# Kernel tuning notes

Hardware: AMD Instinct MI355X
Metric: run time of the kernel (lower is better)

Reference implementation:

```python
import jax, jax.numpy as jnp
import numpy as np

B, T, S, I, H = 128, 256, 256, 512, 512


def setup_inputs() -> dict:
    key = jax.random.key(0)
    ks = jax.random.split(key, 10)
    sc = 0.02
    return {
        "x": jax.random.normal(ks[0], (B, T, I), jnp.float32),
        "h0": jax.random.normal(ks[1], (B, H), jnp.float32),
        "c0": jax.random.normal(ks[2], (B, H), jnp.float32),
        "ctx": jax.random.normal(ks[3], (S, B, H), jnp.float32),
        "Wi": jax.random.normal(ks[4], (4 * H, I), jnp.float32) * sc,
        "bi": jax.random.normal(ks[5], (4 * H,), jnp.float32) * sc,
        "Wh": jax.random.normal(ks[6], (4 * H, H), jnp.float32) * sc,
        "bh": jax.random.normal(ks[7], (4 * H,), jnp.float32) * sc,
        "W_in": jax.random.normal(ks[8], (H, H), jnp.float32) * sc,
        "W_out": jax.random.normal(ks[9], (H, 2 * H), jnp.float32) * sc,
    }


def reference(x, h0, c0, ctx, Wi, bi, Wh, bh, W_in, W_out):
    ctx_b = jnp.transpose(ctx, (1, 0, 2))  # [B, S, H]

    def step(carry, xt):
        hx, cx = carry
        gates = xt @ Wi.T + bi + hx @ Wh.T + bh  # [B, 4H]
        i_g, f_g, g_g, o_g = jnp.split(gates, 4, axis=1)
        cy = jax.nn.sigmoid(f_g) * cx + jax.nn.sigmoid(i_g) * jnp.tanh(g_g)
        hy = jax.nn.sigmoid(o_g) * jnp.tanh(cy)
        # soft dot attention
        target = hy @ W_in.T                              # [B, H]
        attn = jax.nn.softmax(jnp.einsum('bsh,bh->bs', ctx_b, target), axis=1)
        wc = jnp.einsum('bs,bsh->bh', attn, ctx_b)        # [B, H]
        h_tilde = jnp.tanh(jnp.concatenate([wc, hy], axis=1) @ W_out.T)
        return (h_tilde, cy), h_tilde

    (hf, cf), outs = jax.lax.scan(step, (h0, c0), jnp.transpose(x, (1, 0, 2)))
    output = jnp.transpose(outs, (1, 0, 2))  # [B, T, H] (batch_first)
    return output, hf, cf
```

## Files before the change

### kernel.cpp

```cpp
#include <hip/hip_runtime.h>
#include <hip/hip_bf16.h>
#include <stdint.h>

#define B_ 128
#define T_ 256
#define S_ 256
#define I_ 512
#define H_ 512
#define RSLOT 32

typedef __attribute__((ext_vector_type(8))) short short8;
typedef __attribute__((ext_vector_type(4))) float f32x4;
typedef unsigned short ushort_t;

__device__ __forceinline__ float bf2f(ushort_t u){
  union{ unsigned int i; float f;} v; v.i = ((unsigned int)u)<<16; return v.f;
}
__device__ __forceinline__ ushort_t f2bf(float f){
  union{ unsigned int i; float f;} v; v.f=f;
  unsigned int x=v.i; unsigned int r = x + 0x7fffu + ((x>>16)&1u);
  return (ushort_t)(r>>16);
}
__device__ __forceinline__ float sigm(float x){ return 1.f/(1.f + __expf(-x)); }
__device__ __forceinline__ float tanh_s(float x){
  float a = fabsf(x);
  float e = __expf(-2.f*a);
  float t = (1.f - e)/(1.f + e);
  return x < 0.f ? -t : t;
}

__device__ __forceinline__ f32x4 MFMA16(short8 a, short8 b, f32x4 c){
  typedef __attribute__((ext_vector_type(8))) __bf16 bf16x8;
  return __builtin_amdgcn_mfma_f32_16x16x32_bf16(
      __builtin_bit_cast(bf16x8, a), __builtin_bit_cast(bf16x8, b), c, 0, 0, 0);
}

__device__ __forceinline__ void fab_store_u64(ushort_t* p, unsigned long long v){
  __hip_atomic_store((unsigned long long*)p, v, __ATOMIC_RELAXED, __HIP_MEMORY_SCOPE_AGENT);
}


__global__ void k_cvt_bf16(const float* __restrict__ src, ushort_t* __restrict__ dst, int n){
  int i = (blockIdx.x*blockDim.x + threadIdx.x)*4;
  int stride = gridDim.x*blockDim.x*4;
  for (; i < n; i += stride){
    float4 v = *(const float4*)(src + i);
    ushort4 o; o.x=f2bf(v.x); o.y=f2bf(v.y); o.z=f2bf(v.z); o.w=f2bf(v.w);
    *(ushort4*)(dst + i) = o;
  }
}

__global__ void k_relayout_ctx(const float* __restrict__ ctx, ushort_t* __restrict__ ctxb){
  int s = blockIdx.x >> 7;
  int b = blockIdx.x & 127;
  int h4 = threadIdx.x * 4;
  float4 v = *(const float4*)(ctx + ((size_t)s*128 + b)*512 + h4);
  ushort4 o; o.x=f2bf(v.x); o.y=f2bf(v.y); o.z=f2bf(v.z); o.w=f2bf(v.w);
  *(ushort4*)(ctxb + ((size_t)b*256 + s)*512 + h4) = o;
}

__global__ void k_transpose_512(const float* __restrict__ in, float* __restrict__ out){
  __shared__ float tile[32][33];
  int bx = blockIdx.x*32, by = blockIdx.y*32;
  int tx = threadIdx.x, ty = threadIdx.y;
  for (int r=0;r<32;r+=8) tile[ty+r][tx] = in[(by+ty+r)*512 + bx+tx];
  __syncthreads();
  for (int r=0;r<32;r+=8) out[(bx+ty+r)*512 + by+tx] = tile[tx][ty+r];
}

__global__ void k_init_state(const float* __restrict__ h0, const float* __restrict__ c0,
                             ushort_t* __restrict__ hring0, float* __restrict__ cyb){
  int i = blockIdx.x*blockDim.x + threadIdx.x;
  hring0[i] = f2bf(h0[i]);
  cyb[i] = c0[i];
}

__global__ void k_zero_bar(int* f){
  if (threadIdx.x < 256) f[threadIdx.x] = 0;
}

template<int BIAS, int SWAP>
__global__ __launch_bounds__(256) void k_gemm_bt(
    const float* __restrict__ A, const float* __restrict__ Bm,
    ushort_t* __restrict__ C, int M, int N, int K,
    const float* __restrict__ bias0, const float* __restrict__ bias1){
  __shared__ ushort_t Asm[128][40];
  __shared__ ushort_t Bsm[128][40];
  const int tid = threadIdx.x;
  const int mBase = blockIdx.x*128, nBase = blockIdx.y*128;
  const int l = tid & 63, wv = tid >> 6;
  const int wm = (wv>>1)*64, wn = (wv&1)*64;
  const int lr = l & 15, lq = l >> 4;
  const int srow = tid >> 1, scol = (tid & 1)*16;
  const float* Ap = A + (size_t)(mBase + srow)*K + scol;
  const float* Bp = Bm + (size_t)(nBase + srow)*K + scol;

  f32x4 acc[4][4];
  #pragma unroll
  for (int i=0;i<4;i++)
    #pragma unroll
    for (int j=0;j<4;j++) acc[i][j] = (f32x4)0.f;

  for (int k0 = 0; k0 < K; k0 += 32){
    float4 a0 = *(const float4*)(Ap + k0);
    float4 a1 = *(const float4*)(Ap + k0 + 4);
    float4 a2 = *(const float4*)(Ap + k0 + 8);
    float4 a3 = *(const float4*)(Ap + k0 + 12);
    float4 b0 = *(const float4*)(Bp + k0);
    float4 b1 = *(const float4*)(Bp + k0 + 4);
    float4 b2 = *(const float4*)(Bp + k0 + 8);
    float4 b3 = *(const float4*)(Bp + k0 + 12);
    __syncthreads();
    {
      ushort4 w;
      w.x=f2bf(a0.x); w.y=f2bf(a0.y); w.z=f2bf(a0.z); w.w=f2bf(a0.w);
      *(ushort4*)&Asm[srow][scol+0]  = w;
      w.x=f2bf(a1.x); w.y=f2bf(a1.y); w.z=f2bf(a1.z); w.w=f2bf(a1.w);
      *(ushort4*)&Asm[srow][scol+4]  = w;
      w.x=f2bf(a2.x); w.y=f2bf(a2.y); w.z=f2bf(a2.z); w.w=f2bf(a2.w);
      *(ushort4*)&Asm[srow][scol+8]  = w;
      w.x=f2bf(a3.x); w.y=f2bf(a3.y); w.z=f2bf(a3.z); w.w=f2bf(a3.w);
      *(ushort4*)&Asm[srow][scol+12] = w;
      w.x=f2bf(b0.x); w.y=f2bf(b0.y); w.z=f2bf(b0.z); w.w=f2bf(b0.w);
      *(ushort4*)&Bsm[srow][scol+0]  = w;
      w.x=f2bf(b1.x); w.y=f2bf(b1.y); w.z=f2bf(b1.z); w.w=f2bf(b1.w);
      *(ushort4*)&Bsm[srow][scol+4]  = w;
      w.x=f2bf(b2.x); w.y=f2bf(b2.y); w.z=f2bf(b2.z); w.w=f2bf(b2.w);
      *(ushort4*)&Bsm[srow][scol+8]  = w;
      w.x=f2bf(b3.x); w.y=f2bf(b3.y); w.z=f2bf(b3.z); w.w=f2bf(b3.w);
      *(ushort4*)&Bsm[srow][scol+12] = w;
    }
    __syncthreads();
    short8 aF[4], bF[4];
    #pragma unroll
    for (int i=0;i<4;i++) aF[i] = *(const short8*)&Asm[wm + i*16 + lr][lq*8];
    #pragma unroll
    for (int j=0;j<4;j++) bF[j] = *(const short8*)&Bsm[wn + j*16 + lr][lq*8];
    #pragma unroll
    for (int i=0;i<4;i++)
      #pragma unroll
      for (int j=0;j<4;j++)
        acc[i][j] = MFMA16(aF[i], bF[j], acc[i][j]);
  }

  #pragma unroll
  for (int j=0;j<4;j++){
    int col = nBase + wn + j*16 + lr;
    float bsum = 0.f;
    if (BIAS) bsum = bias0[col] + bias1[col];
    #pragma unroll
    for (int i=0;i<4;i++){
      int row0 = mBase + wm + i*16 + lq*4;
      #pragma unroll
      for (int r=0;r<4;r++){
        int row = row0 + r;
        size_t drow = SWAP ? ((size_t)(row & 127)*256 + (row >> 7)) : (size_t)row;
        C[drow*N + col] = f2bf(acc[i][j][r] + bsum);
      }
    }
  }
}

__device__ __forceinline__ void gbar(int* flags, int gen){
  __syncthreads();
  const int tid = threadIdx.x;
  if (tid == 0)
    __hip_atomic_store(&flags[blockIdx.x], gen, __ATOMIC_RELAXED, __HIP_MEMORY_SCOPE_AGENT);
  if (tid < 256){
    while (__hip_atomic_load(&flags[tid], __ATOMIC_RELAXED, __HIP_MEMORY_SCOPE_AGENT) < gen)
      __builtin_amdgcn_s_sleep(2);
  }
  __syncthreads();
  asm volatile("" ::: "memory");
}


__global__ __launch_bounds__(512) void k_persist(
    const ushort_t* __restrict__ Xg, const ushort_t* __restrict__ C2b,
    const ushort_t* __restrict__ ctxb, const ushort_t* __restrict__ Whb,
    const ushort_t* __restrict__ Woutb,
    ushort_t* hring, ushort_t* hyring, ushort_t* wcring,
    float* cyb, float* out, float* hf, float* cf, int* flags)
{
  __shared__ union {
    struct { float red[8][256]; ushort_t pk[256]; } a;
    struct { float sc[256]; float p[256]; float inv;
             float pacc[16][256]; ushort_t pk[256]; } b;
  } sh;

  const int pbid = blockIdx.x;
  const int tid = threadIdx.x;
  const int l = tid & 63, wv = tid >> 6;
  const int lr = l & 15, lq = l >> 4;

  const int bm = pbid >> 5, hc = pbid & 31;
  const int gate = wv & 3, khalf = wv >> 2;
  short8 whr[8];
  #pragma unroll
  for (int kk=0;kk<8;kk++)
    whr[kk] = *(const short8*)(Whb + (size_t)(gate*512 + hc*16 + lr)*512
                               + khalf*256 + lq*8 + kk*32);
  short8 wor[4];
  #pragma unroll
  for (int kk=0;kk<4;kk++)
    wor[kk] = *(const short8*)(Woutb + (size_t)(hc*16 + lr)*1024
                               + wv*128 + lq*8 + kk*32);

  const int bB = pbid >> 1, half = pbid & 1;

  int gen = 0;
  for (int t = 0; t < T_; ++t){
    const size_t slotC = (size_t)(t & (RSLOT-1)) * 65536;

    {
      f32x4 acc = (f32x4)0.f;
      const ushort_t* ap = hring + slotC + (size_t)(bm*16 + lr)*512 + khalf*256 + lq*8;
      short8 hv8[8];
      #pragma unroll
      for (int kk=0;kk<8;kk++) hv8[kk] = *(const short8*)(ap + kk*32);
      #pragma unroll
      for (int kk=0;kk<8;kk++) acc = MFMA16(hv8[kk], whr[kk], acc);
      #pragma unroll
      for (int r=0;r<4;r++) sh.a.red[wv][(lq*4+r)*16+lr] = acc[r];
      __syncthreads();
      if (tid < 256){
        const int b = bm*16 + (tid>>4), h = hc*16 + (tid&15);
        const ushort_t* xg = Xg + ((size_t)b*T_ + t)*2048 + h;
        float gi  = sh.a.red[0][tid] + sh.a.red[4][tid] + bf2f(xg[0]);
        float gf  = sh.a.red[1][tid] + sh.a.red[5][tid] + bf2f(xg[512]);
        float gg  = sh.a.red[2][tid] + sh.a.red[6][tid] + bf2f(xg[1024]);
        float go_ = sh.a.red[3][tid] + sh.a.red[7][tid] + bf2f(xg[1536]);
        float co = cyb[b*512 + h];
        float cn = sigm(gf)*co + sigm(gi)*tanh_s(gg);
        float hn = sigm(go_)*tanh_s(cn);
        cyb[b*512 + h] = cn;
        sh.a.pk[tid] = f2bf(hn);
        if (t == T_-1) cf[b*512 + h] = cn;
      }
      __syncthreads();
      if (tid < 64){
        unsigned long long v = *(unsigned long long*)&sh.a.pk[tid*4];
        fab_store_u64(hyring + slotC + (size_t)(bm*16 + (tid>>2))*512
                      + hc*16 + (tid&3)*4, v);
      }
    }
    gbar(flags, ++gen);

    {
      float hv[8];
      {
        short8 hvv = *(const short8*)(hyring + slotC + (size_t)bB*512 + l*8);
        #pragma unroll
        for (int e=0;e<8;e++) hv[e] = bf2f((ushort_t)hvv[e]);
      }
      {
        const ushort_t* c2p = C2b + (size_t)bB*131072 + (size_t)(wv*32)*512 + l*8;
        short8 ca[8], cb[8];
        #pragma unroll
        for (int j=0;j<8;j++) ca[j] = *(const short8*)(c2p + (size_t)j*512);
        #pragma unroll
        for (int c=0;c<4;c++){
          if (c<3){
            #pragma unroll
            for (int j=0;j<8;j++){
              short8 v = *(const short8*)(c2p + (size_t)((c+1)*8+j)*512);
              if (c&1) ca[j]=v; else cb[j]=v;
            }
          }
          #pragma unroll
          for (int j=0;j<8;j++){
            short8 cv = (c&1)? cb[j] : ca[j];
            float d = 0.f;
            #pragma unroll
            for (int e=0;e<8;e++) d += bf2f((ushort_t)cv[e]) * hv[e];
            #pragma unroll
            for (int off=32; off; off>>=1) d += __shfl_xor(d, off);
            if (l==0) sh.b.sc[wv*32 + c*8 + j] = d;
          }
        }
      }
      __syncthreads();
      if (wv == 0){
        float v0=sh.b.sc[l], v1=sh.b.sc[l+64], v2=sh.b.sc[l+128], v3=sh.b.sc[l+192];
        float m = fmaxf(fmaxf(v0,v1), fmaxf(v2,v3));
        #pragma unroll
        for (int off=32; off; off>>=1) m = fmaxf(m, __shfl_xor(m, off));
        float e0=__expf(v0-m), e1=__expf(v1-m), e2=__expf(v2-m), e3=__expf(v3-m);
        float s4 = (e0+e1)+(e2+e3);
        #pragma unroll
        for (int off=32; off; off>>=1) s4 += __shfl_xor(s4, off);
        sh.b.p[l]=e0; sh.b.p[l+64]=e1; sh.b.p[l+128]=e2; sh.b.p[l+192]=e3;
        if (l==0) sh.b.inv = 1.f/s4;
      }
      __syncthreads();
      {
        const int g = tid & 31, p = tid >> 5;
        const ushort_t* cxp = ctxb + ((size_t)bB*256 + p*16)*512 + half*256 + g*8;
        short8 va[8], vb[8];
        #pragma unroll
        for (int j=0;j<8;j++) va[j] = *(const short8*)(cxp + (size_t)j*512);
        #pragma unroll
        for (int j=0;j<8;j++) vb[j] = *(const short8*)(cxp + (size_t)(8+j)*512);
        float a8[8];
        #pragma unroll
        for (int e=0;e<8;e++) a8[e]=0.f;
        #pragma unroll
        for (int j=0;j<8;j++){
          float pw = sh.b.p[p*16 + j];
          #pragma unroll
          for (int e=0;e<8;e++) a8[e] += pw * bf2f((ushort_t)va[j][e]);
        }
        #pragma unroll
        for (int j=0;j<8;j++){
          float pw = sh.b.p[p*16 + 8 + j];
          #pragma unroll
          for (int e=0;e<8;e++) a8[e] += pw * bf2f((ushort_t)vb[j][e]);
        }
        #pragma unroll
        for (int e=0;e<8;e++) sh.b.pacc[p][g*8+e] = a8[e];
      }
      __syncthreads();
      if (tid < 256){
        float s = 0.f;
        #pragma unroll
        for (int p2=0;p2<16;p2++) s += sh.b.pacc[p2][tid];
        sh.b.pk[tid] = f2bf(s * sh.b.inv);
      }
      __syncthreads();
      if (tid < 64){
        unsigned long long v = *(unsigned long long*)&sh.b.pk[tid*4];
        fab_store_u64(wcring + slotC + (size_t)bB*512 + half*256 + tid*4, v);
      }
    }
    gbar(flags, ++gen);

    {
      f32x4 acc = (f32x4)0.f;
      const ushort_t* ap = (wv < 4 ? wcring : hyring) + slotC
                           + (size_t)(bm*16 + lr)*512 + (wv&3)*128 + lq*8;
      short8 av[4];
      #pragma unroll
      for (int kk=0;kk<4;kk++) av[kk] = *(const short8*)(ap + kk*32);
      #pragma unroll
      for (int kk=0;kk<4;kk++) acc = MFMA16(av[kk], wor[kk], acc);
      #pragma unroll
      for (int r=0;r<4;r++) sh.a.red[wv][(lq*4+r)*16+lr] = acc[r];
      __syncthreads();
      if (tid < 256){
        float s = 0.f;
        #pragma unroll
        for (int w=0;w<8;w++) s += sh.a.red[w][tid];
        float v = tanh_s(s);
        const int b = bm*16 + (tid>>4), n = hc*16 + (tid&15);
        out[((size_t)b*T_ + t)*512 + n] = v;
        sh.a.pk[tid] = f2bf(v);
        if (t == T_-1) hf[b*512 + n] = v;
      }
      __syncthreads();
      if (tid < 64){
        unsigned long long v = *(unsigned long long*)&sh.a.pk[tid*4];
        size_t slotN = (size_t)((t+1) & (RSLOT-1)) * 65536;
        fab_store_u64(hring + slotN + (size_t)(bm*16 + (tid>>2))*512
                      + hc*16 + (tid&3)*4, v);
      }
    }
    gbar(flags, ++gen);
  }
}


extern "C" void kernel_launch(void* const* d_in, const int* in_sizes, int n_in,
                              void* d_out, int out_size, void* d_ws, size_t ws_size,
                              hipStream_t stream){
  const float* x    = (const float*)d_in[0];
  const float* h0   = (const float*)d_in[1];
  const float* c0   = (const float*)d_in[2];
  const float* ctx  = (const float*)d_in[3];
  const float* Wi   = (const float*)d_in[4];
  const float* bi   = (const float*)d_in[5];
  const float* Wh   = (const float*)d_in[6];
  const float* bh   = (const float*)d_in[7];
  const float* Win  = (const float*)d_in[8];
  const float* Wout = (const float*)d_in[9];

  char* ws = (char*)d_ws;
  ushort_t* Xg     = (ushort_t*)(ws);
  ushort_t* C2b    = (ushort_t*)(ws + 134217728);
  ushort_t* ctxb   = (ushort_t*)(ws + 167772160);
  ushort_t* Whb    = (ushort_t*)(ws + 201326592);
  ushort_t* Woutb  = (ushort_t*)(ws + 203423744);
  float*    WinT   = (float*)   (ws + 204472320);
  ushort_t* hring  = (ushort_t*)(ws + 205520896);
  ushort_t* hyring = (ushort_t*)(ws + 209715200);
  ushort_t* wcring = (ushort_t*)(ws + 213909504);
  float*    cyb    = (float*)   (ws + 218103808);
  int*      flags  = (int*)     (ws + 218365952);

  float* out = (float*)d_out;
  float* hf  = out + (size_t)B_*T_*H_;
  float* cf  = hf + (size_t)B_*H_;

  k_relayout_ctx<<<32768, 128, 0, stream>>>(ctx, ctxb);
  k_cvt_bf16<<<512, 256, 0, stream>>>(Wh, Whb, 4*H_*H_);
  k_cvt_bf16<<<512, 256, 0, stream>>>(Wout, Woutb, H_*2*H_);
  k_transpose_512<<<dim3(16,16), dim3(32,8), 0, stream>>>(Win, WinT);
  k_init_state<<<256, 256, 0, stream>>>(h0, c0, hring, cyb);
  k_zero_bar<<<1, 256, 0, stream>>>(flags);

  k_gemm_bt<1,0><<<dim3(256,16), 256, 0, stream>>>(x, Wi, Xg, B_*T_, 4*H_, I_, bi, bh);
  k_gemm_bt<0,1><<<dim3(256,4), 256, 0, stream>>>(ctx, WinT, C2b, S_*B_, H_, H_, nullptr, nullptr);

  k_persist<<<256, 512, 0, stream>>>(Xg, C2b, ctxb, Whb, Woutb,
                                     hring, hyring, wcring,
                                     cyb, out, hf, cf, flags);
}
```

Measured before the change: 9.044 ms.

## Keep ctx resident in LDS and compute attention target per step

Drops the precomputed ctx·W_in GEMM and the global ctx relayout. Each persistent block now converts its 256x256 slice of ctx to bf16 once and keeps it in swizzled LDS (128KB dynamic). Every step computes target = W_in·hy, takes partial scores against the LDS copy, and swaps half-sums with its buddy block through a global mailbox. This removes the per-step global reads of C2b and ctxb, but adds a third grid barrier per timestep plus a per-step W_in matvec read from global memory. The Xg and cy loads are also hoisted ahead of the recurrent MFMA.

```diff
diff --git a/kernel.cpp b/kernel.cpp
--- a/kernel.cpp
+++ b/kernel.cpp
@@ -12,6 +12,7 @@
 typedef __attribute__((ext_vector_type(8))) short short8;
 typedef __attribute__((ext_vector_type(4))) float f32x4;
 typedef unsigned short ushort_t;
+typedef unsigned long long u64;
 
 __device__ __forceinline__ float bf2f(ushort_t u){
   union{ unsigned int i; float f;} v; v.i = ((unsigned int)u)<<16; return v.f;
@@ -35,8 +36,8 @@
       __builtin_bit_cast(bf16x8, a), __builtin_bit_cast(bf16x8, b), c, 0, 0, 0);
 }
 
-__device__ __forceinline__ void fab_store_u64(ushort_t* p, unsigned long long v){
-  __hip_atomic_store((unsigned long long*)p, v, __ATOMIC_RELAXED, __HIP_MEMORY_SCOPE_AGENT);
+__device__ __forceinline__ void fab_store_u64(void* p, u64 v){
+  __hip_atomic_store((u64*)p, v, __ATOMIC_RELAXED, __HIP_MEMORY_SCOPE_AGENT);
 }
 
 
@@ -50,24 +51,6 @@
   }
 }
 
-__global__ void k_relayout_ctx(const float* __restrict__ ctx, ushort_t* __restrict__ ctxb){
-  int s = blockIdx.x >> 7;
-  int b = blockIdx.x & 127;
-  int h4 = threadIdx.x * 4;
-  float4 v = *(const float4*)(ctx + ((size_t)s*128 + b)*512 + h4);
-  ushort4 o; o.x=f2bf(v.x); o.y=f2bf(v.y); o.z=f2bf(v.z); o.w=f2bf(v.w);
-  *(ushort4*)(ctxb + ((size_t)b*256 + s)*512 + h4) = o;
-}
-
-__global__ void k_transpose_512(const float* __restrict__ in, float* __restrict__ out){
-  __shared__ float tile[32][33];
-  int bx = blockIdx.x*32, by = blockIdx.y*32;
-  int tx = threadIdx.x, ty = threadIdx.y;
-  for (int r=0;r<32;r+=8) tile[ty+r][tx] = in[(by+ty+r)*512 + bx+tx];
-  __syncthreads();
-  for (int r=0;r<32;r+=8) out[(bx+ty+r)*512 + by+tx] = tile[tx][ty+r];
-}
-
 __global__ void k_init_state(const float* __restrict__ h0, const float* __restrict__ c0,
                              ushort_t* __restrict__ hring0, float* __restrict__ cyb){
   int i = blockIdx.x*blockDim.x + threadIdx.x;
@@ -76,10 +59,9 @@
 }
 
 __global__ void k_zero_bar(int* f){
-  if (threadIdx.x < 256) f[threadIdx.x] = 0;
-}
-
-template<int BIAS, int SWAP>
+  f[threadIdx.x] = 0;
+}
+
 __global__ __launch_bounds__(256) void k_gemm_bt(
     const float* __restrict__ A, const float* __restrict__ Bm,
     ushort_t* __restrict__ C, int M, int N, int K,
@@ -146,17 +128,13 @@
   #pragma unroll
   for (int j=0;j<4;j++){
     int col = nBase + wn + j*16 + lr;
-    float bsum = 0.f;
-    if (BIAS) bsum = bias0[col] + bias1[col];
+    float bsum = bias0[col] + bias1[col];
     #pragma unroll
     for (int i=0;i<4;i++){
       int row0 = mBase + wm + i*16 + lq*4;
       #pragma unroll
-      for (int r=0;r<4;r++){
-        int row = row0 + r;
-        size_t drow = SWAP ? ((size_t)(row & 127)*256 + (row >> 7)) : (size_t)row;
-        C[drow*N + col] = f2bf(acc[i][j][r] + bsum);
-      }
+      for (int r=0;r<4;r++)
+        C[(size_t)(row0+r)*N + col] = f2bf(acc[i][j][r] + bsum);
     }
   }
 }
@@ -176,15 +154,19 @@
 
 
 __global__ __launch_bounds__(512) void k_persist(
-    const ushort_t* __restrict__ Xg, const ushort_t* __restrict__ C2b,
-    const ushort_t* __restrict__ ctxb, const ushort_t* __restrict__ Whb,
-    const ushort_t* __restrict__ Woutb,
+    const ushort_t* __restrict__ Xg, const float* __restrict__ ctx,
+    const ushort_t* __restrict__ Whb, const ushort_t* __restrict__ Woutb,
+    const ushort_t* __restrict__ Winb,
     ushort_t* hring, ushort_t* hyring, ushort_t* wcring,
-    float* cyb, float* out, float* hf, float* cf, int* flags)
+    float* cyb, float* psmail, float* out, float* hf, float* cf,
+    int* flags)
 {
-  __shared__ union {
+  extern __shared__ __align__(16) char ctx_s[];
+
+  __shared__ __align__(16) union {
     struct { float red[8][256]; ushort_t pk[256]; } a;
-    struct { float sc[256]; float p[256]; float inv;
+    struct { float hy[512]; float tg[256]; float ps[256]; float sc[256];
+             float p[256]; float inv; float pad;
              float pacc[16][256]; ushort_t pk[256]; } b;
   } sh;
 
@@ -208,11 +190,32 @@
 
   const int bB = pbid >> 1, half = pbid & 1;
 
+  {
+    const float* cp = ctx + (size_t)bB*512 + half*256 + (tid & 63)*4;
+    #pragma unroll 4
+    for (int i = 0; i < 32; ++i){
+      int s = i*8 + (tid >> 6);
+      float4 v = *(const float4*)(cp + (size_t)s*65536);
+      ushort4 o; o.x=f2bf(v.x); o.y=f2bf(v.y); o.z=f2bf(v.z); o.w=f2bf(v.w);
+      int boff = ((tid & 63)*8) ^ ((s & 7) << 4);
+      *(ushort4*)(ctx_s + s*512 + boff) = o;
+    }
+  }
+  __syncthreads();
+
   int gen = 0;
   for (int t = 0; t < T_; ++t){
     const size_t slotC = (size_t)(t & (RSLOT-1)) * 65536;
+    const int slotI = t & (RSLOT-1);
 
     {
+      ushort_t x0=0,x1=0,x2=0,x3=0; float co = 0.f;
+      if (tid < 256){
+        const int b = bm*16 + (tid>>4), h = hc*16 + (tid&15);
+        const ushort_t* xg = Xg + ((size_t)b*T_ + t)*2048 + h;
+        x0 = xg[0]; x1 = xg[512]; x2 = xg[1024]; x3 = xg[1536];
+        co = cyb[b*512 + h];
+      }
       f32x4 acc = (f32x4)0.f;
       const ushort_t* ap = hring + slotC + (size_t)(bm*16 + lr)*512 + khalf*256 + lq*8;
       short8 hv8[8];
@@ -225,12 +228,10 @@
       __syncthreads();
       if (tid < 256){
         const int b = bm*16 + (tid>>4), h = hc*16 + (tid&15);
-        const ushort_t* xg = Xg + ((size_t)b*T_ + t)*2048 + h;
-        float gi  = sh.a.red[0][tid] + sh.a.red[4][tid] + bf2f(xg[0]);
-        float gf  = sh.a.red[1][tid] + sh.a.red[5][tid] + bf2f(xg[512]);
-        float gg  = sh.a.red[2][tid] + sh.a.red[6][tid] + bf2f(xg[1024]);
-        float go_ = sh.a.red[3][tid] + sh.a.red[7][tid] + bf2f(xg[1536]);
-        float co = cyb[b*512 + h];
+        float gi  = sh.a.red[0][tid] + sh.a.red[4][tid] + bf2f(x0);
+        float gf  = sh.a.red[1][tid] + sh.a.red[5][tid] + bf2f(x1);
+        float gg  = sh.a.red[2][tid] + sh.a.red[6][tid] + bf2f(x2);
+        float go_ = sh.a.red[3][tid] + sh.a.red[7][tid] + bf2f(x3);
         float cn = sigm(gf)*co + sigm(gi)*tanh_s(gg);
         float hn = sigm(go_)*tanh_s(cn);
         cyb[b*512 + h] = cn;
@@ -239,7 +240,7 @@
       }
       __syncthreads();
       if (tid < 64){
-        unsigned long long v = *(unsigned long long*)&sh.a.pk[tid*4];
+        u64 v = *(u64*)&sh.a.pk[tid*4];
         fab_store_u64(hyring + slotC + (size_t)(bm*16 + (tid>>2))*512
                       + hc*16 + (tid&3)*4, v);
       }
@@ -247,36 +248,56 @@
     gbar(flags, ++gen);
 
     {
-      float hv[8];
+      if (tid < 128){
+        ushort4 v = *(const ushort4*)(hyring + slotC + (size_t)bB*512 + tid*4);
+        sh.b.hy[tid*4+0]=bf2f(v.x); sh.b.hy[tid*4+1]=bf2f(v.y);
+        sh.b.hy[tid*4+2]=bf2f(v.z); sh.b.hy[tid*4+3]=bf2f(v.w);
+      }
+      __syncthreads();
       {
-        short8 hvv = *(const short8*)(hyring + slotC + (size_t)bB*512 + l*8);
-        #pragma unroll
-        for (int e=0;e<8;e++) hv[e] = bf2f((ushort_t)hvv[e]);
-      }
+        const int j = tid >> 1, kh = tid & 1;
+        const ushort_t* wp = Winb + (size_t)(half*256 + j)*512 + kh*256;
+        float d = 0.f;
+        #pragma unroll
+        for (int c = 0; c < 32; ++c){
+          short8 w8 = *(const short8*)(wp + c*8);
+          #pragma unroll
+          for (int e=0;e<8;e++) d += bf2f((ushort_t)w8[e]) * sh.b.hy[kh*256 + c*8 + e];
+        }
+        d += __shfl_xor(d, 1);
+        if (kh == 0) sh.b.tg[j] = d;
+      }
+      __syncthreads();
       {
-        const ushort_t* c2p = C2b + (size_t)bB*131072 + (size_t)(wv*32)*512 + l*8;
-        short8 ca[8], cb[8];
-        #pragma unroll
-        for (int j=0;j<8;j++) ca[j] = *(const short8*)(c2p + (size_t)j*512);
-        #pragma unroll
-        for (int c=0;c<4;c++){
-          if (c<3){
-            #pragma unroll
-            for (int j=0;j<8;j++){
-              short8 v = *(const short8*)(c2p + (size_t)((c+1)*8+j)*512);
-              if (c&1) ca[j]=v; else cb[j]=v;
-            }
-          }
+        const int s = tid >> 1, qh = tid & 1;
+        const int swz = (s & 7) << 4;
+        float d = 0.f;
+        #pragma unroll
+        for (int c = 0; c < 16; ++c){
+          int eb = c*16 + qh*8;
+          short8 cv = *(const short8*)(ctx_s + s*512 + ((eb*2) ^ swz));
           #pragma unroll
-          for (int j=0;j<8;j++){
-            short8 cv = (c&1)? cb[j] : ca[j];
-            float d = 0.f;
-            #pragma unroll
-            for (int e=0;e<8;e++) d += bf2f((ushort_t)cv[e]) * hv[e];
-            #pragma unroll
-            for (int off=32; off; off>>=1) d += __shfl_xor(d, off);
-            if (l==0) sh.b.sc[wv*32 + c*8 + j] = d;
-          }
+          for (int e=0;e<8;e++) d += bf2f((ushort_t)cv[e]) * sh.b.tg[eb + e];
+        }
+        d += __shfl_xor(d, 1);
+        if (qh == 0) sh.b.ps[s] = d;
+      }
+      __syncthreads();
+      {
+        float* mymail = psmail + ((size_t)(bB*2 + half)*RSLOT + slotI)*256;
+        if (tid < 128)
+          fab_store_u64(mymail + tid*2, *(u64*)&sh.b.ps[tid*2]);
+      }
+    }
+    gbar(flags, ++gen);
+
+    {
+      {
+        const float* budp = psmail + ((size_t)(bB*2 + (half^1))*RSLOT + slotI)*256;
+        if (tid < 128){
+          float2 f2 = *(const float2*)(budp + tid*2);
+          sh.b.sc[tid*2]   = sh.b.ps[tid*2]   + f2.x;
+          sh.b.sc[tid*2+1] = sh.b.ps[tid*2+1] + f2.y;
         }
       }
       __syncthreads();
@@ -295,40 +316,30 @@
       __syncthreads();
       {
         const int g = tid & 31, p = tid >> 5;
-        const ushort_t* cxp = ctxb + ((size_t)bB*256 + p*16)*512 + half*256 + g*8;
-        short8 va[8], vb[8];
-        #pragma unroll
-        for (int j=0;j<8;j++) va[j] = *(const short8*)(cxp + (size_t)j*512);
-        #pragma unroll
-        for (int j=0;j<8;j++) vb[j] = *(const short8*)(cxp + (size_t)(8+j)*512);
         float a8[8];
         #pragma unroll
         for (int e=0;e<8;e++) a8[e]=0.f;
         #pragma unroll
-        for (int j=0;j<8;j++){
-          float pw = sh.b.p[p*16 + j];
+        for (int j=0;j<16;j++){
+          int s = p*16 + j;
+          short8 cv = *(const short8*)(ctx_s + s*512 + ((g*16) ^ ((s&7)<<4)));
+          float pw = sh.b.p[s];
           #pragma unroll
-          for (int e=0;e<8;e++) a8[e] += pw * bf2f((ushort_t)va[j][e]);
+          for (int e=0;e<8;e++) a8[e] += pw * bf2f((ushort_t)cv[e]);
         }
         #pragma unroll
-        for (int j=0;j<8;j++){
-          float pw = sh.b.p[p*16 + 8 + j];
-          #pragma unroll
-          for (int e=0;e<8;e++) a8[e] += pw * bf2f((ushort_t)vb[j][e]);
-        }
-        #pragma unroll
         for (int e=0;e<8;e++) sh.b.pacc[p][g*8+e] = a8[e];
       }
       __syncthreads();
       if (tid < 256){
-        float s = 0.f;
-        #pragma unroll
-        for (int p2=0;p2<16;p2++) s += sh.b.pacc[p2][tid];
-        sh.b.pk[tid] = f2bf(s * sh.b.inv);
+        float ssum = 0.f;
+        #pragma unroll
+        for (int p2=0;p2<16;p2++) ssum += sh.b.pacc[p2][tid];
+        sh.b.pk[tid] = f2bf(ssum * sh.b.inv);
       }
       __syncthreads();
       if (tid < 64){
-        unsigned long long v = *(unsigned long long*)&sh.b.pk[tid*4];
+        u64 v = *(u64*)&sh.b.pk[tid*4];
         fab_store_u64(wcring + slotC + (size_t)bB*512 + half*256 + tid*4, v);
       }
     }
@@ -358,7 +369,7 @@
       }
       __syncthreads();
       if (tid < 64){
-        unsigned long long v = *(unsigned long long*)&sh.a.pk[tid*4];
+        u64 v = *(u64*)&sh.a.pk[tid*4];
         size_t slotN = (size_t)((t+1) & (RSLOT-1)) * 65536;
         fab_store_u64(hring + slotN + (size_t)(bm*16 + (tid>>2))*512
                       + hc*16 + (tid&3)*4, v);
@@ -385,32 +396,33 @@
 
   char* ws = (char*)d_ws;
   ushort_t* Xg     = (ushort_t*)(ws);
-  ushort_t* C2b    = (ushort_t*)(ws + 134217728);
-  ushort_t* ctxb   = (ushort_t*)(ws + 167772160);
-  ushort_t* Whb    = (ushort_t*)(ws + 201326592);
-  ushort_t* Woutb  = (ushort_t*)(ws + 203423744);
-  float*    WinT   = (float*)   (ws + 204472320);
-  ushort_t* hring  = (ushort_t*)(ws + 205520896);
-  ushort_t* hyring = (ushort_t*)(ws + 209715200);
-  ushort_t* wcring = (ushort_t*)(ws + 213909504);
-  float*    cyb    = (float*)   (ws + 218103808);
-  int*      flags  = (int*)     (ws + 218365952);
+  ushort_t* Whb    = (ushort_t*)(ws + 134217728);
+  ushort_t* Woutb  = (ushort_t*)(ws + 136314880);
+  ushort_t* Winb   = (ushort_t*)(ws + 137363456);
+  ushort_t* hring  = (ushort_t*)(ws + 137887744);
+  ushort_t* hyring = (ushort_t*)(ws + 142082048);
+  ushort_t* wcring = (ushort_t*)(ws + 146276352);
+  float*    cyb    = (float*)   (ws + 150470656);
+  float*    psmail = (float*)   (ws + 150732800);
+  int*      flags  = (int*)     (ws + 159121408);
 
   float* out = (float*)d_out;
   float* hf  = out + (size_t)B_*T_*H_;
   float* cf  = hf + (size_t)B_*H_;
 
-  k_relayout_ctx<<<32768, 128, 0, stream>>>(ctx, ctxb);
+  hipFuncSetAttribute((const void*)k_persist,
+                      hipFuncAttributeMaxDynamicSharedMemorySize, 131072);
+
   k_cvt_bf16<<<512, 256, 0, stream>>>(Wh, Whb, 4*H_*H_);
   k_cvt_bf16<<<512, 256, 0, stream>>>(Wout, Woutb, H_*2*H_);
-  k_transpose_512<<<dim3(16,16), dim3(32,8), 0, stream>>>(Win, WinT);
+  k_cvt_bf16<<<256, 256, 0, stream>>>(Win, Winb, H_*H_);
   k_init_state<<<256, 256, 0, stream>>>(h0, c0, hring, cyb);
   k_zero_bar<<<1, 256, 0, stream>>>(flags);
 
-  k_gemm_bt<1,0><<<dim3(256,16), 256, 0, stream>>>(x, Wi, Xg, B_*T_, 4*H_, I_, bi, bh);
-  k_gemm_bt<0,1><<<dim3(256,4), 256, 0, stream>>>(ctx, WinT, C2b, S_*B_, H_, H_, nullptr, nullptr);
-
-  k_persist<<<256, 512, 0, stream>>>(Xg, C2b, ctxb, Whb, Woutb,
-                                     hring, hyring, wcring,
-                                     cyb, out, hf, cf, flags);
-}
+  k_gemm_bt<<<dim3(256,16), 256, 0, stream>>>(x, Wi, Xg, B_*T_, 4*H_, I_, bi, bh);
+
+  k_persist<<<256, 512, 131072, stream>>>(Xg, ctx, Whb, Woutb, Winb,
+                                          hring, hyring, wcring,
+                                          cyb, psmail, out, hf, cf,
+                                          flags);
+}
```

Measured after the change: 10.32 ms. 14.1% more time.
